# Kernel optimization log

Measured on AMD Instinct MI355X. Metric: run time of the kernel, lower is better.

Reference implementation:

```python
import jax, jax.numpy as jnp
import numpy as np

N_NODES = 2048


def setup_inputs() -> dict:
    key = jax.random.key(0)
    ks = jax.random.split(key, 9)
    N, IN, HID, OUT, R, B1 = N_NODES, 64, 32, 16, 4, 1
    s = 0.1
    return {
        "x": jax.random.normal(ks[0], (N, IN), jnp.float32),
        # adj_initial = ones - eye, as in __init__ (learnable parameter)
        "adj_matrix": jnp.ones((N, N), jnp.float32) - jnp.eye(N, dtype=jnp.float32),
        "bases1": jax.random.normal(ks[1], (B1, IN, HID), jnp.float32) * s,
        "coeff1": jax.random.normal(ks[2], (R, B1), jnp.float32) * s,
        "loop_w1": jax.random.normal(ks[3], (IN, HID), jnp.float32) * s,
        "bias1": jnp.zeros((HID,), jnp.float32),
        "bases2": jax.random.normal(ks[4], (R, HID, OUT), jnp.float32) * s,
        "coeff2": jax.random.normal(ks[5], (R, R), jnp.float32) * s,
        "loop_w2": jax.random.normal(ks[6], (HID, OUT), jnp.float32) * s,
        "bias2": jnp.zeros((OUT,), jnp.float32),
        "edge_type": 0,  # ignored by the module (etype is rebuilt as zeros)
    }


def _rel_graph_conv(h, bases, coeff, loop_w, bias, src, dst, n_nodes, act):
    # basis regularizer: W_r = sum_b coeff[r, b] * bases[b]; all edges have etype 0
    W0 = jnp.einsum('b,bio->io', coeff[0], bases)          # [in, out]
    msg = (h @ W0)[src]                                    # [E, out] gather-by-edge
    agg = jax.ops.segment_sum(msg, dst, num_segments=n_nodes)  # scatter-sum
    out = agg + h @ loop_w + bias                          # self-loop + bias
    return act(out)


def reference(x, adj_matrix, bases1, coeff1, loop_w1, bias1,
              bases2, coeff2, loop_w2, bias2, edge_type):
    N = x.shape[0]
    # sigmoid(adj_matrix) > 0 everywhere (sigmoid(0)=0.5 on the diagonal), so
    # torch.nonzero yields ALL N^2 pairs in row-major order: complete graph
    # with self-loops. Structure is static -> build edges with arange.
    idx = jnp.arange(N)
    src = jnp.repeat(idx, N)   # [N*N]
    dst = jnp.tile(idx, N)     # [N*N]
    h = _rel_graph_conv(x, bases1, coeff1, loop_w1, bias1, src, dst, N, jax.nn.relu)
    h = _rel_graph_conv(h, bases2, coeff2, loop_w2, bias2, src, dst, N, lambda z: z)
    return h
```

## Files before the change

kernel.cpp:

```cpp
#include <hip/hip_runtime.h>

#define NN   2048
#define IN   64
#define HID  32
#define OUTD 16

#define S0P 0
#define H1O 4096
#define S1P (4096 + NN * HID)

__global__ __launch_bounds__(256) void k1_colsum_x(const float* __restrict__ x,
                                                   float* __restrict__ ws) {
    __shared__ float red[256];
    const int tid = threadIdx.x, b = blockIdx.x;
    const int col = tid & 63, grp = tid >> 6;
    const float* xb = x + b * 32 * IN;
    float s = 0.f;
#pragma unroll
    for (int r = 0; r < 8; ++r)
        s += xb[(grp * 8 + r) * IN + col];
    red[tid] = s;
    __syncthreads();
    if (tid < 64)
        ws[S0P + b * 64 + tid] = red[tid] + red[tid + 64] + red[tid + 128] + red[tid + 192];
}

__global__ __launch_bounds__(256) void k2_layer1(const float* __restrict__ x,
                                                 const float* __restrict__ bases1,
                                                 const float* __restrict__ coeff1,
                                                 const float* __restrict__ loop_w1,
                                                 const float* __restrict__ bias1,
                                                 float* __restrict__ ws) {
    __shared__ float w1sh[IN * HID];
    __shared__ float xsh[32 * IN];
    __shared__ float s0sh[IN];
    __shared__ float agg1sh[HID];
    __shared__ float red[256];
    const int tid = threadIdx.x, b = blockIdx.x;

    const float4* x4  = (const float4*)(x + b * 32 * IN);
    const float4* w14 = (const float4*)loop_w1;
    float4 xa = x4[tid], xb4 = x4[tid + 256];
    float4 wa = w14[tid], wb = w14[tid + 256];

    {
        const int col = tid & 63, g = tid >> 6;
        float a0 = 0.f, a1 = 0.f, a2 = 0.f, a3 = 0.f;
#pragma unroll
        for (int k = 0; k < 4; ++k) {
            a0 += ws[S0P + (g * 16 + k     ) * 64 + col];
            a1 += ws[S0P + (g * 16 + 4 + k ) * 64 + col];
            a2 += ws[S0P + (g * 16 + 8 + k ) * 64 + col];
            a3 += ws[S0P + (g * 16 + 12 + k) * 64 + col];
        }
        ((float4*)xsh)[tid] = xa; ((float4*)xsh)[tid + 256] = xb4;
        ((float4*)w1sh)[tid] = wa; ((float4*)w1sh)[tid + 256] = wb;
        red[tid] = a0 + a1 + a2 + a3;
    }
    __syncthreads();
    if (tid < 64)
        s0sh[tid] = red[tid] + red[tid + 64] + red[tid + 128] + red[tid + 192];
    __syncthreads();

    {
        const int h = tid & 31, seg = tid >> 5;
        float p = 0.f;
#pragma unroll
        for (int k = 0; k < 8; ++k)
            p += s0sh[seg * 8 + k] * bases1[(seg * 8 + k) * HID + h];
        red[tid] = p;
        __syncthreads();
        if (tid < HID) {
            float t = 0.f;
#pragma unroll
            for (int g = 0; g < 8; ++g) t += red[g * 32 + tid];
            agg1sh[tid] = bias1[tid] + coeff1[0] * t;
        }
    }
    __syncthreads();

    {
        const int h = tid & 31, rgrp = tid >> 5;
        const float agg1v = agg1sh[h];
        float a0 = agg1v, a1 = agg1v, a2 = agg1v, a3 = agg1v;
#pragma unroll
        for (int k = 0; k < IN; ++k) {
            const float w = w1sh[k * HID + h];
            a0 += xsh[(rgrp +  0) * IN + k] * w;
            a1 += xsh[(rgrp +  8) * IN + k] * w;
            a2 += xsh[(rgrp + 16) * IN + k] * w;
            a3 += xsh[(rgrp + 24) * IN + k] * w;
        }
        a0 = fmaxf(a0, 0.f); a1 = fmaxf(a1, 0.f);
        a2 = fmaxf(a2, 0.f); a3 = fmaxf(a3, 0.f);
        float* h1b = ws + H1O + b * 32 * HID;
        h1b[(rgrp +  0) * HID + h] = a0;
        h1b[(rgrp +  8) * HID + h] = a1;
        h1b[(rgrp + 16) * HID + h] = a2;
        h1b[(rgrp + 24) * HID + h] = a3;
        red[tid] = a0 + a1 + a2 + a3;
    }
    __syncthreads();
    if (tid < HID) {
        float t = 0.f;
#pragma unroll
        for (int g = 0; g < 8; ++g) t += red[g * 32 + tid];
        ws[S1P + b * HID + tid] = t;
    }
}

__global__ __launch_bounds__(256) void k3_layer2(const float* __restrict__ bases2,
                                                 const float* __restrict__ coeff2,
                                                 const float* __restrict__ loop_w2,
                                                 const float* __restrict__ bias2,
                                                 const float* __restrict__ ws,
                                                 float* __restrict__ out) {
    __shared__ float w2sh[HID * OUTD];
    __shared__ float w2csh[HID * OUTD];
    __shared__ float h1sh[16 * (HID + 1)];
    __shared__ float s1sh[HID];
    __shared__ float agg2sh[OUTD];
    __shared__ float red[256];
    const int tid = threadIdx.x, b = blockIdx.x;

    {
        const float c20 = coeff2[0], c21 = coeff2[1], c22 = coeff2[2], c23 = coeff2[3];
#pragma unroll
        for (int j = 0; j < 2; ++j) {
            const int i = tid + j * 256;
            w2sh[i]  = loop_w2[i];
            w2csh[i] = c20 * bases2[i]        + c21 * bases2[512 + i] +
                       c22 * bases2[1024 + i] + c23 * bases2[1536 + i];
        }
    }
    for (int j = 0; j < 2; ++j) {
        const int i = tid + j * 256;
        h1sh[(i >> 5) * (HID + 1) + (i & 31)] = ws[H1O + b * 16 * HID + i];
    }
    {
        const int h = tid & 31, g = tid >> 5;
        float a0 = 0.f, a1 = 0.f;
#pragma unroll
        for (int k = 0; k < 4; ++k) {
            a0 += ws[S1P + (g * 8 + k    ) * HID + h];
            a1 += ws[S1P + (g * 8 + 4 + k) * HID + h];
        }
        red[tid] = a0 + a1;
    }
    __syncthreads();
    if (tid < HID) {
        float t = 0.f;
#pragma unroll
        for (int g = 0; g < 8; ++g) t += red[g * 32 + tid];
        s1sh[tid] = t;
    }
    __syncthreads();
    if (tid < OUTD) {
        float s = 0.f;
#pragma unroll
        for (int h = 0; h < HID; ++h) s += s1sh[h] * w2csh[h * OUTD + tid];
        agg2sh[tid] = bias2[tid] + s;
    }
    __syncthreads();

    {
        const int row = tid >> 4, o = tid & 15;
        float acc = agg2sh[o];
#pragma unroll
        for (int h = 0; h < HID; ++h)
            acc += h1sh[row * (HID + 1) + h] * w2sh[h * OUTD + o];
        out[b * 256 + tid] = acc;
    }
}

extern "C" void kernel_launch(void* const* d_in, const int* in_sizes, int n_in,
                              void* d_out, int out_size, void* d_ws, size_t ws_size,
                              hipStream_t stream) {
    const float* x       = (const float*)d_in[0];
    const float* bases1  = (const float*)d_in[2];
    const float* coeff1  = (const float*)d_in[3];
    const float* loop_w1 = (const float*)d_in[4];
    const float* bias1   = (const float*)d_in[5];
    const float* bases2  = (const float*)d_in[6];
    const float* coeff2  = (const float*)d_in[7];
    const float* loop_w2 = (const float*)d_in[8];
    const float* bias2   = (const float*)d_in[9];
    float* out = (float*)d_out;
    float* ws  = (float*)d_ws;

    k1_colsum_x<<<64, 256, 0, stream>>>(x, ws);
    k2_layer1 <<<64, 256, 0, stream>>>(x, bases1, coeff1, loop_w1, bias1, ws);
    k3_layer2 <<<128, 256, 0, stream>>>(bases2, coeff2, loop_w2, bias2, ws, out);
}
```

Measured before the change: 90.08 us.

## Fuse column-sum passes into layer kernels, dropping one launch

Removes the separate column-sum kernel. Each layer-1 block now redundantly reduces all of x (2048x64) to get the column sum, and each layer-2 block redundantly reduces all of h1 instead of reading per-block partial sums. Layer 2 now runs 64 blocks, each handling 32 rows with two accumulators per thread. This trades a kernel launch and its inter-kernel dependency for redundant global reads (512 KB per block for x, 256 KB per block for h1), which mostly hit L2.

```diff
diff --git a/kernel.cpp b/kernel.cpp
--- a/kernel.cpp
+++ b/kernel.cpp
@@ -5,37 +5,19 @@
 #define HID  32
 #define OUTD 16
 
-#define S0P 0
-#define H1O 4096
-#define S1P (4096 + NN * HID)
 
-__global__ __launch_bounds__(256) void k1_colsum_x(const float* __restrict__ x,
-                                                   float* __restrict__ ws) {
-    __shared__ float red[256];
-    const int tid = threadIdx.x, b = blockIdx.x;
-    const int col = tid & 63, grp = tid >> 6;
-    const float* xb = x + b * 32 * IN;
-    float s = 0.f;
-#pragma unroll
-    for (int r = 0; r < 8; ++r)
-        s += xb[(grp * 8 + r) * IN + col];
-    red[tid] = s;
-    __syncthreads();
-    if (tid < 64)
-        ws[S0P + b * 64 + tid] = red[tid] + red[tid + 64] + red[tid + 128] + red[tid + 192];
-}
-
-__global__ __launch_bounds__(256) void k2_layer1(const float* __restrict__ x,
+__global__ __launch_bounds__(256) void kA_layer1(const float* __restrict__ x,
                                                  const float* __restrict__ bases1,
                                                  const float* __restrict__ coeff1,
                                                  const float* __restrict__ loop_w1,
                                                  const float* __restrict__ bias1,
                                                  float* __restrict__ ws) {
-    __shared__ float w1sh[IN * HID];
-    __shared__ float xsh[32 * IN];
-    __shared__ float s0sh[IN];
-    __shared__ float agg1sh[HID];
-    __shared__ float red[256];
+    __shared__ float  w1sh[IN * HID];
+    __shared__ float  xsh[32 * IN];
+    __shared__ float4 red4[256];
+    __shared__ float  red[256];
+    __shared__ float  s0sh[IN];
+    __shared__ float  agg1sh[HID];
     const int tid = threadIdx.x, b = blockIdx.x;
 
     const float4* x4  = (const float4*)(x + b * 32 * IN);
@@ -44,22 +26,29 @@
     float4 wa = w14[tid], wb = w14[tid + 256];
 
     {
-        const int col = tid & 63, g = tid >> 6;
-        float a0 = 0.f, a1 = 0.f, a2 = 0.f, a3 = 0.f;
-#pragma unroll
-        for (int k = 0; k < 4; ++k) {
-            a0 += ws[S0P + (g * 16 + k     ) * 64 + col];
-            a1 += ws[S0P + (g * 16 + 4 + k ) * 64 + col];
-            a2 += ws[S0P + (g * 16 + 8 + k ) * 64 + col];
-            a3 += ws[S0P + (g * 16 + 12 + k) * 64 + col];
+        const int q = tid & 15, rg = tid >> 4;
+        const float4* xg = (const float4*)x;
+        float4 s = {0.f, 0.f, 0.f, 0.f};
+#pragma unroll 8
+        for (int r = rg; r < NN; r += 16) {
+            float4 v = xg[r * 16 + q];
+            s.x += v.x; s.y += v.y; s.z += v.z; s.w += v.w;
         }
         ((float4*)xsh)[tid] = xa; ((float4*)xsh)[tid + 256] = xb4;
         ((float4*)w1sh)[tid] = wa; ((float4*)w1sh)[tid + 256] = wb;
-        red[tid] = a0 + a1 + a2 + a3;
+        red4[tid] = s;
     }
     __syncthreads();
-    if (tid < 64)
-        s0sh[tid] = red[tid] + red[tid + 64] + red[tid + 128] + red[tid + 192];
+    if (tid < 16) {
+        float4 t = {0.f, 0.f, 0.f, 0.f};
+#pragma unroll
+        for (int g = 0; g < 16; ++g) {
+            float4 v = red4[g * 16 + tid];
+            t.x += v.x; t.y += v.y; t.z += v.z; t.w += v.w;
+        }
+        s0sh[tid * 4 + 0] = t.x; s0sh[tid * 4 + 1] = t.y;
+        s0sh[tid * 4 + 2] = t.z; s0sh[tid * 4 + 3] = t.w;
+    }
     __syncthreads();
 
     {
@@ -93,34 +82,26 @@
         }
         a0 = fmaxf(a0, 0.f); a1 = fmaxf(a1, 0.f);
         a2 = fmaxf(a2, 0.f); a3 = fmaxf(a3, 0.f);
-        float* h1b = ws + H1O + b * 32 * HID;
+        float* h1b = ws + b * 32 * HID;
         h1b[(rgrp +  0) * HID + h] = a0;
         h1b[(rgrp +  8) * HID + h] = a1;
         h1b[(rgrp + 16) * HID + h] = a2;
         h1b[(rgrp + 24) * HID + h] = a3;
-        red[tid] = a0 + a1 + a2 + a3;
-    }
-    __syncthreads();
-    if (tid < HID) {
-        float t = 0.f;
-#pragma unroll
-        for (int g = 0; g < 8; ++g) t += red[g * 32 + tid];
-        ws[S1P + b * HID + tid] = t;
     }
 }
 
-__global__ __launch_bounds__(256) void k3_layer2(const float* __restrict__ bases2,
+__global__ __launch_bounds__(256) void kB_layer2(const float* __restrict__ bases2,
                                                  const float* __restrict__ coeff2,
                                                  const float* __restrict__ loop_w2,
                                                  const float* __restrict__ bias2,
                                                  const float* __restrict__ ws,
                                                  float* __restrict__ out) {
-    __shared__ float w2sh[HID * OUTD];
-    __shared__ float w2csh[HID * OUTD];
-    __shared__ float h1sh[16 * (HID + 1)];
-    __shared__ float s1sh[HID];
-    __shared__ float agg2sh[OUTD];
-    __shared__ float red[256];
+    __shared__ float  w2sh[HID * OUTD];
+    __shared__ float  w2csh[HID * OUTD];
+    __shared__ float  h1sh[32 * 36];
+    __shared__ float4 red4[256];
+    __shared__ float  s1sh[HID];
+    __shared__ float  agg2sh[OUTD];
     const int tid = threadIdx.x, b = blockIdx.x;
 
     {
@@ -133,26 +114,32 @@
                        c22 * bases2[1024 + i] + c23 * bases2[1536 + i];
         }
     }
-    for (int j = 0; j < 2; ++j) {
-        const int i = tid + j * 256;
-        h1sh[(i >> 5) * (HID + 1) + (i & 31)] = ws[H1O + b * 16 * HID + i];
+    {
+        const float4 v = ((const float4*)(ws + b * 32 * HID))[tid];
+        const int row = tid >> 3, q = tid & 7;
+        ((float4*)&h1sh[row * 36])[q] = v;
     }
     {
-        const int h = tid & 31, g = tid >> 5;
-        float a0 = 0.f, a1 = 0.f;
-#pragma unroll
-        for (int k = 0; k < 4; ++k) {
-            a0 += ws[S1P + (g * 8 + k    ) * HID + h];
-            a1 += ws[S1P + (g * 8 + 4 + k) * HID + h];
+        const int q = tid & 7, rg = tid >> 3;
+        const float4* hg = (const float4*)ws;
+        float4 s = {0.f, 0.f, 0.f, 0.f};
+#pragma unroll 8
+        for (int r = rg; r < NN; r += 32) {
+            float4 v = hg[r * 8 + q];
+            s.x += v.x; s.y += v.y; s.z += v.z; s.w += v.w;
         }
-        red[tid] = a0 + a1;
+        red4[tid] = s;
     }
     __syncthreads();
-    if (tid < HID) {
-        float t = 0.f;
+    if (tid < 8) {
+        float4 t = {0.f, 0.f, 0.f, 0.f};
 #pragma unroll
-        for (int g = 0; g < 8; ++g) t += red[g * 32 + tid];
-        s1sh[tid] = t;
+        for (int g = 0; g < 32; ++g) {
+            float4 v = red4[g * 8 + tid];
+            t.x += v.x; t.y += v.y; t.z += v.z; t.w += v.w;
+        }
+        s1sh[tid * 4 + 0] = t.x; s1sh[tid * 4 + 1] = t.y;
+        s1sh[tid * 4 + 2] = t.z; s1sh[tid * 4 + 3] = t.w;
     }
     __syncthreads();
     if (tid < OUTD) {
@@ -164,12 +151,16 @@
     __syncthreads();
 
     {
-        const int row = tid >> 4, o = tid & 15;
-        float acc = agg2sh[o];
+        const int r0 = tid >> 4, o = tid & 15;
+        float acc0 = agg2sh[o], acc1 = agg2sh[o];
 #pragma unroll
-        for (int h = 0; h < HID; ++h)
-            acc += h1sh[row * (HID + 1) + h] * w2sh[h * OUTD + o];
-        out[b * 256 + tid] = acc;
+        for (int h = 0; h < HID; ++h) {
+            const float w = w2sh[h * OUTD + o];
+            acc0 += h1sh[(r0     ) * 36 + h] * w;
+            acc1 += h1sh[(r0 + 16) * 36 + h] * w;
+        }
+        out[b * 512 + tid]       = acc0;
+        out[b * 512 + 256 + tid] = acc1;
     }
 }
 
@@ -188,7 +179,6 @@
     float* out = (float*)d_out;
     float* ws  = (float*)d_ws;
 
-    k1_colsum_x<<<64, 256, 0, stream>>>(x, ws);
-    k2_layer1 <<<64, 256, 0, stream>>>(x, bases1, coeff1, loop_w1, bias1, ws);
-    k3_layer2 <<<128, 256, 0, stream>>>(bases2, coeff2, loop_w2, bias2, ws, out);
+    kA_layer1<<<64, 256, 0, stream>>>(x, bases1, coeff1, loop_w1, bias1, ws);
+    kB_layer2<<<64, 256, 0, stream>>>(bases2, coeff2, loop_w2, bias2, ws, out);
 }
```

New measurement: 96.69 us. 1.07x slower.

## Fuse layer-2 self-loop matmul into layer-1 kernel, keep h1 in shared memory

Applied to the files above, without the earlier changes.

Layer 1 now keeps its hidden activations in shared memory and computes the layer-2 self-loop product (h1 @ loop_w2) directly, writing partial outputs. The global round trip of h1 through the workspace goes away. The final kernel only computes the aggregated column-sum term and adds it to the output in place, which costs an extra read-modify-write of the output. Total work stays about the same, and the three-kernel launch chain is kept.

```diff
diff --git a/kernel.cpp b/kernel.cpp
--- a/kernel.cpp
+++ b/kernel.cpp
@@ -6,8 +6,7 @@
 #define OUTD 16
 
 #define S0P 0
-#define H1O 4096
-#define S1P (4096 + NN * HID)
+#define S1P 4096
 
 __global__ __launch_bounds__(256) void k1_colsum_x(const float* __restrict__ x,
                                                    float* __restrict__ ws) {
@@ -30,9 +29,13 @@
                                                  const float* __restrict__ coeff1,
                                                  const float* __restrict__ loop_w1,
                                                  const float* __restrict__ bias1,
-                                                 float* __restrict__ ws) {
+                                                 const float* __restrict__ loop_w2,
+                                                 float* __restrict__ ws,
+                                                 float* __restrict__ out) {
     __shared__ float w1sh[IN * HID];
     __shared__ float xsh[32 * IN];
+    __shared__ float w2sh[HID * OUTD];
+    __shared__ float h1sh[32 * 33];
     __shared__ float s0sh[IN];
     __shared__ float agg1sh[HID];
     __shared__ float red[256];
@@ -42,6 +45,8 @@
     const float4* w14 = (const float4*)loop_w1;
     float4 xa = x4[tid], xb4 = x4[tid + 256];
     float4 wa = w14[tid], wb = w14[tid + 256];
+    float4 w2v = {0.f, 0.f, 0.f, 0.f};
+    if (tid < 128) w2v = ((const float4*)loop_w2)[tid];
 
     {
         const int col = tid & 63, g = tid >> 6;
@@ -55,6 +60,7 @@
         }
         ((float4*)xsh)[tid] = xa; ((float4*)xsh)[tid + 256] = xb4;
         ((float4*)w1sh)[tid] = wa; ((float4*)w1sh)[tid + 256] = wb;
+        if (tid < 128) ((float4*)w2sh)[tid] = w2v;
         red[tid] = a0 + a1 + a2 + a3;
     }
     __syncthreads();
@@ -93,11 +99,10 @@
         }
         a0 = fmaxf(a0, 0.f); a1 = fmaxf(a1, 0.f);
         a2 = fmaxf(a2, 0.f); a3 = fmaxf(a3, 0.f);
-        float* h1b = ws + H1O + b * 32 * HID;
-        h1b[(rgrp +  0) * HID + h] = a0;
-        h1b[(rgrp +  8) * HID + h] = a1;
-        h1b[(rgrp + 16) * HID + h] = a2;
-        h1b[(rgrp + 24) * HID + h] = a3;
+        h1sh[(rgrp +  0) * 33 + h] = a0;
+        h1sh[(rgrp +  8) * 33 + h] = a1;
+        h1sh[(rgrp + 16) * 33 + h] = a2;
+        h1sh[(rgrp + 24) * 33 + h] = a3;
         red[tid] = a0 + a1 + a2 + a3;
     }
     __syncthreads();
@@ -107,17 +112,26 @@
         for (int g = 0; g < 8; ++g) t += red[g * 32 + tid];
         ws[S1P + b * HID + tid] = t;
     }
-}
-
-__global__ __launch_bounds__(256) void k3_layer2(const float* __restrict__ bases2,
+    {
+        const int r0 = tid >> 4, o = tid & 15;
+        float acc0 = 0.f, acc1 = 0.f;
+#pragma unroll
+        for (int h = 0; h < HID; ++h) {
+            const float w = w2sh[h * OUTD + o];
+            acc0 += h1sh[(r0     ) * 33 + h] * w;
+            acc1 += h1sh[(r0 + 16) * 33 + h] * w;
+        }
+        out[b * 512 + tid]       = acc0;
+        out[b * 512 + 256 + tid] = acc1;
+    }
+}
+
+__global__ __launch_bounds__(256) void k3_finish(const float* __restrict__ bases2,
                                                  const float* __restrict__ coeff2,
-                                                 const float* __restrict__ loop_w2,
                                                  const float* __restrict__ bias2,
                                                  const float* __restrict__ ws,
                                                  float* __restrict__ out) {
-    __shared__ float w2sh[HID * OUTD];
     __shared__ float w2csh[HID * OUTD];
-    __shared__ float h1sh[16 * (HID + 1)];
     __shared__ float s1sh[HID];
     __shared__ float agg2sh[OUTD];
     __shared__ float red[256];
@@ -128,14 +142,9 @@
 #pragma unroll
         for (int j = 0; j < 2; ++j) {
             const int i = tid + j * 256;
-            w2sh[i]  = loop_w2[i];
             w2csh[i] = c20 * bases2[i]        + c21 * bases2[512 + i] +
                        c22 * bases2[1024 + i] + c23 * bases2[1536 + i];
         }
-    }
-    for (int j = 0; j < 2; ++j) {
-        const int i = tid + j * 256;
-        h1sh[(i >> 5) * (HID + 1) + (i & 31)] = ws[H1O + b * 16 * HID + i];
     }
     {
         const int h = tid & 31, g = tid >> 5;
@@ -163,13 +172,13 @@
     }
     __syncthreads();
 
-    {
-        const int row = tid >> 4, o = tid & 15;
-        float acc = agg2sh[o];
-#pragma unroll
-        for (int h = 0; h < HID; ++h)
-            acc += h1sh[row * (HID + 1) + h] * w2sh[h * OUTD + o];
-        out[b * 256 + tid] = acc;
+    if (tid < 128) {
+        const int i = b * 128 + tid;
+        float4 v = ((float4*)out)[i];
+        const int c = (tid & 3) << 2;
+        v.x += agg2sh[c];     v.y += agg2sh[c + 1];
+        v.z += agg2sh[c + 2]; v.w += agg2sh[c + 3];
+        ((float4*)out)[i] = v;
     }
 }
 
@@ -189,6 +198,6 @@
     float* ws  = (float*)d_ws;
 
     k1_colsum_x<<<64, 256, 0, stream>>>(x, ws);
-    k2_layer1 <<<64, 256, 0, stream>>>(x, bases1, coeff1, loop_w1, bias1, ws);
-    k3_layer2 <<<128, 256, 0, stream>>>(bases2, coeff2, loop_w2, bias2, ws, out);
-}
+    k2_layer1 <<<64, 256, 0, stream>>>(x, bases1, coeff1, loop_w1, bias1, loop_w2, ws, out);
+    k3_finish <<<64, 256, 0, stream>>>(bases2, coeff2, bias2, ws, out);
+}
```

Result: no change. 88.35 us (-1.9%).
